# Kernel tuning notes

Measured on AMD Instinct MI355X. Metric: run time of the kernel, lower is better.

Reference implementation:

```python
import jax, jax.numpy as jnp
import numpy as np

N, T, E = 50000, 12, 800000
IN_DIM, SP_DIM, TP_DIM = 128, 128, 128


def setup_inputs() -> dict:
    key = jax.random.key(0)
    ks = jax.random.split(key, 9)
    h = jax.random.normal(ks[0], (N, T, IN_DIM), dtype=jnp.float32)
    src = jax.random.randint(ks[1], (E,), 0, N, dtype=jnp.int32)
    dst = jax.random.randint(ks[2], (E,), 0, N, dtype=jnp.int32)
    s = 1.0 / np.sqrt(IN_DIM).astype(np.float32)
    # GraphConv layer weights (xavier-ish) and zero biases, layer1: in->sp, layer2: sp->sp
    Wg1 = jax.random.normal(ks[3], (IN_DIM, SP_DIM), dtype=jnp.float32) * s
    bg1 = jnp.zeros((SP_DIM,), jnp.float32)
    Wg2 = jax.random.normal(ks[4], (SP_DIM, SP_DIM), dtype=jnp.float32) * s
    bg2 = jnp.zeros((SP_DIM,), jnp.float32)
    # LSTM params, torch layout: [4H, in]/[4H, H], gate order i,f,g,o
    t = 1.0 / np.sqrt(TP_DIM).astype(np.float32)
    w_ih = jax.random.uniform(ks[5], (4 * TP_DIM, IN_DIM), jnp.float32, -t, t)
    w_hh = jax.random.uniform(ks[6], (4 * TP_DIM, TP_DIM), jnp.float32, -t, t)
    b_ih = jax.random.uniform(ks[7], (4 * TP_DIM,), jnp.float32, -t, t)
    b_hh = jax.random.uniform(ks[8], (4 * TP_DIM,), jnp.float32, -t, t)
    return dict(h=h, src=src, dst=dst, Wg1=Wg1, bg1=bg1, Wg2=Wg2, bg2=bg2,
                w_ih=w_ih, w_hh=w_hh, b_ih=b_ih, b_hh=b_hh)


def _graph_conv(x, src, dst, norm_src, norm_dst, W, b):
    # DGL GraphConv norm='both': D_out^{-1/2} on source feats, sum-aggregate to dst,
    # D_in^{-1/2} on result, then dense weight + bias.
    x = x * norm_src                                  # [N, D]
    m = jax.ops.segment_sum(x[src], dst, num_segments=N)  # SpMM: [N, D]
    m = m * norm_dst
    return m @ W + b


def reference(h, src, dst, Wg1, bg1, Wg2, bg2, w_ih, w_hh, b_ih, b_hh):
    ones_e = jnp.ones((E,), jnp.float32)
    out_deg = jnp.maximum(jax.ops.segment_sum(ones_e, src, num_segments=N), 1.0)
    in_deg = jnp.maximum(jax.ops.segment_sum(ones_e, dst, num_segments=N), 1.0)
    norm_src = (out_deg ** -0.5)[:, None]
    norm_dst = (in_deg ** -0.5)[:, None]

    hs_list = []
    for i in range(T):  # fixed small time horizon
        x = h[:, i]  # [N, IN_DIM]
        x = jax.nn.gelu(_graph_conv(x, src, dst, norm_src, norm_dst, Wg1, bg1), approximate=False)
        x = jax.nn.gelu(_graph_conv(x, src, dst, norm_src, norm_dst, Wg2, bg2), approximate=False)
        hs_list.append(jnp.mean(x, axis=0))  # dgl.mean_nodes over the single graph
    hs = jnp.stack(hs_list, axis=0)[None]  # [1, T, SP_DIM]

    # temporal branch: LSTM over time, nodes as batch, then mean over time
    def lstm_step(carry, x_t):
        hp, cp = carry
        gates = x_t @ w_ih.T + b_ih + hp @ w_hh.T + b_hh  # [N, 4H]
        i_, f_, g_, o_ = jnp.split(gates, 4, axis=-1)
        c = jax.nn.sigmoid(f_) * cp + jax.nn.sigmoid(i_) * jnp.tanh(g_)
        ho = jax.nn.sigmoid(o_) * jnp.tanh(c)
        return (ho, c), ho

    h0 = jnp.zeros((N, TP_DIM), jnp.float32)
    _, ht_seq = jax.lax.scan(lstm_step, (h0, h0), jnp.swapaxes(h, 0, 1))  # [T, N, H]
    ht = jnp.mean(ht_seq, axis=0)  # torch.mean over dim=1 (time) -> [N, H]
    return hs, ht
```

## Files before the change

kernel.cpp:

```cpp
#include <hip/hip_runtime.h>
#include <math.h>

#define NN 50000
#define TT 12
#define EE 800000
#define DIM 128

typedef short bf16x8 __attribute__((ext_vector_type(8)));
typedef float f32x4 __attribute__((ext_vector_type(4)));

__device__ __forceinline__ float sigmoidf_(float x) { return 1.0f / (1.0f + expf(-x)); }
__device__ __forceinline__ float geluf_(float x) {
  return 0.5f * x * (1.0f + erff(x * 0.70710678118654752440f));
}
__device__ __forceinline__ unsigned short f2b(float f) {
  union { float f; unsigned u; } v;
  v.f = f;
  unsigned r = (v.u + 0x7fffu + ((v.u >> 16) & 1u)) >> 16;
  return (unsigned short)r;
}
__device__ __forceinline__ float blo(unsigned u) {
  union { unsigned x; float f; } v; v.x = u << 16; return v.f;
}
__device__ __forceinline__ float bhi(unsigned u) {
  union { unsigned x; float f; } v; v.x = u & 0xffff0000u; return v.f;
}
__device__ __forceinline__ float b2f(unsigned short b) {
  union { unsigned u; float f; } v; v.u = ((unsigned)b) << 16; return v.f;
}
__device__ __forceinline__ unsigned short f2h(float f) {
  union { _Float16 h; unsigned short s; } v; v.h = (_Float16)f; return v.s;
}
__device__ __forceinline__ float h2f(unsigned short u) {
  union { unsigned short s; _Float16 h; } v; v.s = u; return (float)v.h;
}


__global__ void deg_kernel(const int* __restrict__ src, const int* __restrict__ dst,
                           int* __restrict__ ds, int* __restrict__ dd) {
  int e = blockIdx.x * 256 + threadIdx.x;
  if (e < EE) {
    atomicAdd(&ds[src[e]], 1);
    atomicAdd(&dd[dst[e]], 1);
  }
}

__global__ void norm_kernel(const int* __restrict__ ds, const int* __restrict__ dd,
                            float* __restrict__ ns, float* __restrict__ nd) {
  int i = blockIdx.x * 256 + threadIdx.x;
  if (i < NN) {
    ns[i] = rsqrtf((float)(ds[i] > 1 ? ds[i] : 1));
    nd[i] = rsqrtf((float)(dd[i] > 1 ? dd[i] : 1));
  }
}

__global__ void scan_kernel(const int* __restrict__ cnt, int* __restrict__ row_ptr, int n) {
  __shared__ int sm[1024];
  __shared__ int carry;
  int tid = threadIdx.x;
  if (tid == 0) carry = 0;
  __syncthreads();
  for (int base = 0; base < n; base += 1024) {
    int v = (base + tid < n) ? cnt[base + tid] : 0;
    sm[tid] = v;
    __syncthreads();
    for (int off = 1; off < 1024; off <<= 1) {
      int t = (tid >= off) ? sm[tid - off] : 0;
      __syncthreads();
      sm[tid] += t;
      __syncthreads();
    }
    int incl = sm[tid];
    if (base + tid < n) row_ptr[base + tid] = carry + incl - v;
    int tot = sm[1023];
    __syncthreads();
    if (tid == 0) carry += tot;
    __syncthreads();
  }
  if (tid == 0) row_ptr[n] = carry;
}

__global__ void csr_kernel(const int* __restrict__ src, const int* __restrict__ dst,
                           const int* __restrict__ row_ptr, int* __restrict__ fill,
                           int* __restrict__ col) {
  int e = blockIdx.x * 256 + threadIdx.x;
  if (e < EE) {
    int d = dst[e];
    int pos = row_ptr[d] + atomicAdd(&fill[d], 1);
    col[pos] = src[e];
  }
}


__global__ void prep_w(const float* __restrict__ Wg1, const float* __restrict__ Wg2,
                       const float* __restrict__ wih, const float* __restrict__ whh,
                       const float* __restrict__ bih, const float* __restrict__ bhh,
                       unsigned short* __restrict__ W2bt, unsigned short* __restrict__ Wcomb,
                       unsigned short* __restrict__ whhb, float* __restrict__ bgate) {
  int i = blockIdx.x * 256 + threadIdx.x;
  if (i < 16384) {
    int n = i >> 7, k = i & 127;
    W2bt[i] = f2b(Wg2[k * 128 + n]);
  }
  int j = i - 16384;
  if (j >= 0 && j < 81920) {
    int n = j >> 7, k = j & 127;
    Wcomb[j] = f2b(n < 128 ? Wg1[k * 128 + n] : wih[(n - 128) * 128 + k]);
  }
  int q = i - (16384 + 81920);
  if (q >= 0 && q < 65536) whhb[q] = f2b(whh[q]);
  if (i < 512) bgate[i] = bih[i] + bhh[i];
}

#define LDT 40

__global__ __launch_bounds__(256) void gemm_h_all(
    const float* __restrict__ A, const float* __restrict__ ns,
    const unsigned short* __restrict__ Wcomb, unsigned short* __restrict__ C,
    unsigned short* __restrict__ xg, int M) {
  __shared__ unsigned short As[4 * 128 * LDT];
  __shared__ unsigned short Bs[128 * LDT];
  const int tid = threadIdx.x;
  const int lane = tid & 63, wid = tid >> 6;
  const int quad = lane >> 4, l16 = lane & 15;
  const int row0 = blockIdx.x * 128;
  const int wm = (wid >> 1) * 64, wn = (wid & 1) * 64;

#pragma unroll
  for (int rds = 0; rds < 8; rds++) {
    int idx = rds * 256 + tid;
    int m = idx >> 4;
    int k8 = (idx & 15) * 8;
    int gr = row0 + m;
    if (gr >= M) gr = M - 1;
    const float4 va = *(const float4*)(A + (size_t)gr * 128 + k8);
    const float4 vb = *(const float4*)(A + (size_t)gr * 128 + k8 + 4);
    int chunk = k8 >> 5, c = k8 & 31;
    unsigned short* d = &As[(chunk * 128 + m) * LDT + c];
    d[0] = f2b(va.x); d[1] = f2b(va.y); d[2] = f2b(va.z); d[3] = f2b(va.w);
    d[4] = f2b(vb.x); d[5] = f2b(vb.y); d[6] = f2b(vb.z); d[7] = f2b(vb.w);
  }

  for (int cb = 0; cb < 5; cb++) {
    f32x4 acc[4][4] = {};
#pragma unroll
    for (int k0 = 0; k0 < 4; k0++) {
      __syncthreads();
      {
        int n = tid >> 1;
        int c = (tid & 1) * 16;
        const unsigned short* srcw = Wcomb + ((size_t)(cb * 128 + n)) * 128 + k0 * 32 + c;
        *(uint4*)(&Bs[n * LDT + c]) = *(const uint4*)srcw;
        *(uint4*)(&Bs[n * LDT + c + 8]) = *(const uint4*)(srcw + 8);
      }
      __syncthreads();
      bf16x8 af[4], bfr[4];
#pragma unroll
      for (int im = 0; im < 4; im++)
        af[im] = *(const bf16x8*)(&As[(k0 * 128 + wm + im * 16 + l16) * LDT + quad * 8]);
#pragma unroll
      for (int in = 0; in < 4; in++)
        bfr[in] = *(const bf16x8*)(&Bs[(wn + in * 16 + l16) * LDT + quad * 8]);
#pragma unroll
      for (int im = 0; im < 4; im++)
#pragma unroll
        for (int in = 0; in < 4; in++)
          acc[im][in] = __builtin_amdgcn_mfma_f32_16x16x32_bf16(af[im], bfr[in], acc[im][in], 0, 0, 0);
    }
    if (cb == 0) {
#pragma unroll
      for (int im = 0; im < 4; im++)
#pragma unroll
        for (int r = 0; r < 4; r++) {
          int row = row0 + wm + im * 16 + quad * 4 + r;
          if (row < M) {
            float s = ns[row / TT];
#pragma unroll
            for (int in = 0; in < 4; in++)
              C[(size_t)row * 128 + wn + in * 16 + l16] = f2b(acc[im][in][r] * s);
          }
        }
    } else {
      const int goff = (cb - 1) * 128;
#pragma unroll
      for (int im = 0; im < 4; im++)
#pragma unroll
        for (int r = 0; r < 4; r++) {
          int row = row0 + wm + im * 16 + quad * 4 + r;
          if (row < M)
#pragma unroll
            for (int in = 0; in < 4; in++)
              xg[(size_t)row * 512 + goff + wn + in * 16 + l16] = f2h(acc[im][in][r]);
        }
    }
  }
}

__global__ __launch_bounds__(256) void gemm_bf16A(
    const unsigned short* __restrict__ A, const unsigned short* __restrict__ Bt,
    unsigned short* __restrict__ C, int M) {
  __shared__ unsigned short As[128 * LDT];
  __shared__ unsigned short Bs[128 * LDT];
  const int tid = threadIdx.x;
  const int lane = tid & 63, wid = tid >> 6;
  const int quad = lane >> 4, l16 = lane & 15;
  const int row0 = blockIdx.x * 128;
  const int wm = (wid >> 1) * 64, wn = (wid & 1) * 64;
  f32x4 acc[4][4] = {};
  for (int k0 = 0; k0 < 128; k0 += 32) {
#pragma unroll
    for (int rds = 0; rds < 2; rds++) {
      int idx = (rds * 256 + tid) * 8;
      int m = idx >> 5, c = idx & 31;
      int gr = row0 + m;
      if (gr >= M) gr = M - 1;
      *(uint4*)(&As[m * LDT + c]) = *(const uint4*)(A + (size_t)gr * 128 + k0 + c);
      *(uint4*)(&Bs[m * LDT + c]) = *(const uint4*)(Bt + m * 128 + k0 + c);
    }
    __syncthreads();
    bf16x8 af[4], bfr[4];
#pragma unroll
    for (int im = 0; im < 4; im++)
      af[im] = *(const bf16x8*)(&As[(wm + im * 16 + l16) * LDT + quad * 8]);
#pragma unroll
    for (int in = 0; in < 4; in++)
      bfr[in] = *(const bf16x8*)(&Bs[(wn + in * 16 + l16) * LDT + quad * 8]);
#pragma unroll
    for (int im = 0; im < 4; im++)
#pragma unroll
      for (int in = 0; in < 4; in++)
        acc[im][in] = __builtin_amdgcn_mfma_f32_16x16x32_bf16(af[im], bfr[in], acc[im][in], 0, 0, 0);
    __syncthreads();
  }
#pragma unroll
  for (int im = 0; im < 4; im++)
#pragma unroll
    for (int r = 0; r < 4; r++) {
      int row = row0 + wm + im * 16 + quad * 4 + r;
      if (row < M)
#pragma unroll
        for (int in = 0; in < 4; in++)
          C[(size_t)row * 128 + wn + in * 16 + l16] = f2b(acc[im][in][r]);
    }
}


template <bool SCALE_OUT>
__global__ __launch_bounds__(256) void spmm_b(
    const unsigned short* __restrict__ z, const int* __restrict__ rowp,
    const int* __restrict__ colx, const float* __restrict__ ns,
    const float* __restrict__ nd, const float* __restrict__ bg,
    unsigned short* __restrict__ y) {
  int d = (blockIdx.x * 256 + threadIdx.x) >> 6;
  int lane = threadIdx.x & 63;
  if (d >= NN) return;
  int beg = rowp[d], end = rowp[d + 1];
  float acc[3][8] = {};
  int j = beg;
  int s = (j < end) ? colx[j] : 0;
  while (j < end) {
    int snext = (j + 1 < end) ? colx[j + 1] : 0;
    const unsigned short* base = z + (size_t)s * 1536 + lane * 8;
#pragma unroll
    for (int r = 0; r < 3; r++) {
      uint4 v = *(const uint4*)(base + r * 512);
      acc[r][0] += blo(v.x); acc[r][1] += bhi(v.x);
      acc[r][2] += blo(v.y); acc[r][3] += bhi(v.y);
      acc[r][4] += blo(v.z); acc[r][5] += bhi(v.z);
      acc[r][6] += blo(v.w); acc[r][7] += bhi(v.w);
    }
    s = snext;
    j++;
  }
  float scn = nd[d];
  float sco = SCALE_OUT ? ns[d] : 1.0f;
  float bgv[8];
#pragma unroll
  for (int k = 0; k < 8; k++) bgv[k] = bg[(lane * 8 + k) & 127];
  unsigned short* outp = y + (size_t)d * 1536 + lane * 8;
#pragma unroll
  for (int r = 0; r < 3; r++) {
    unsigned short o[8];
#pragma unroll
    for (int k = 0; k < 8; k++)
      o[k] = f2b(sco * geluf_(acc[r][k] * scn + bgv[k]));
    *(uint4*)(outp + r * 512) = *(const uint4*)o;
  }
}


__global__ void colmean_b(const unsigned short* __restrict__ x, float* __restrict__ out) {
  int t = blockIdx.x;
  int cc = threadIdx.x & 127;
  int half = threadIdx.x >> 7;
  float s = 0.f;
  for (int n = blockIdx.y * 2 + half; n < NN; n += 64)
    s += b2f(x[((size_t)n * TT + t) * 128 + cc]);
  __shared__ float sm[256];
  sm[threadIdx.x] = s;
  __syncthreads();
  if (threadIdx.x < 128)
    atomicAdd(&out[t * 128 + cc], (sm[threadIdx.x] + sm[threadIdx.x + 128]) * (1.0f / NN));
}

#define HPLD 136
#define WLD 136

__global__ __launch_bounds__(512, 2) void lstm_hh(
    const unsigned short* __restrict__ whhb, const unsigned short* __restrict__ xg,
    const float* __restrict__ bgate, float* __restrict__ ht_out, int M) {
  __shared__ unsigned short Ws[512 * WLD];
  __shared__ unsigned short Hp[64 * HPLD];
  const int tid = threadIdx.x;
  const int lane = tid & 63;
  const int w = tid >> 6;
  const int quad = lane >> 4, l16 = lane & 15;
  const int row0 = blockIdx.x * 64;
  const int colg = w * 16 + l16;

#pragma unroll
  for (int it = 0; it < 16; it++) {
    int idx = it * 512 + tid;
    int n = idx >> 4, c = (idx & 15) * 8;
    *(uint4*)(&Ws[n * WLD + c]) = *(const uint4*)(whhb + n * 128 + c);
  }

  float cs[4][4], hacc[4][4];
#pragma unroll
  for (int im = 0; im < 4; im++)
#pragma unroll
    for (int r = 0; r < 4; r++) { cs[im][r] = 0.f; hacc[im][r] = 0.f; }

  const float bi = bgate[colg], bff = bgate[128 + colg];
  const float bgg = bgate[256 + colg], bo = bgate[384 + colg];
  __syncthreads();

  for (int t = 0; t < TT; t++) {
    unsigned short xsv[4][4][4];
#pragma unroll
    for (int im = 0; im < 4; im++)
#pragma unroll
      for (int r = 0; r < 4; r++) {
        int gr = row0 + im * 16 + quad * 4 + r;
        int grc = gr < M ? gr : M - 1;
        const unsigned short* xp = xg + ((size_t)grc * TT + t) * 512 + colg;
#pragma unroll
        for (int g = 0; g < 4; g++) xsv[im][r][g] = xp[g * 128];
      }

    f32x4 acc[4][4] = {};
    if (t) {
#pragma unroll
      for (int k0 = 0; k0 < 128; k0 += 32) {
        bf16x8 af[4];
#pragma unroll
        for (int im = 0; im < 4; im++)
          af[im] = *(const bf16x8*)(&Hp[(im * 16 + l16) * HPLD + k0 + quad * 8]);
#pragma unroll
        for (int g = 0; g < 4; g++) {
          bf16x8 bf = *(const bf16x8*)(&Ws[(g * 128 + colg) * WLD + k0 + quad * 8]);
#pragma unroll
          for (int im = 0; im < 4; im++)
            acc[im][g] = __builtin_amdgcn_mfma_f32_16x16x32_bf16(af[im], bf, acc[im][g], 0, 0, 0);
        }
      }
      __syncthreads();
    }

#pragma unroll
    for (int im = 0; im < 4; im++)
#pragma unroll
      for (int r = 0; r < 4; r++) {
        float iv = sigmoidf_(acc[im][0][r] + h2f(xsv[im][r][0]) + bi);
        float fv = sigmoidf_(acc[im][1][r] + h2f(xsv[im][r][1]) + bff);
        float gv = tanhf(acc[im][2][r] + h2f(xsv[im][r][2]) + bgg);
        float ov = sigmoidf_(acc[im][3][r] + h2f(xsv[im][r][3]) + bo);
        float cn = fv * cs[im][r] + iv * gv;
        cs[im][r] = cn;
        float ho = ov * tanhf(cn);
        hacc[im][r] += ho;
        Hp[(im * 16 + quad * 4 + r) * HPLD + colg] = f2b(ho);
      }
    __syncthreads();
  }
#pragma unroll
  for (int im = 0; im < 4; im++)
#pragma unroll
    for (int r = 0; r < 4; r++) {
      int gr = row0 + im * 16 + quad * 4 + r;
      if (gr < M) ht_out[(size_t)gr * 128 + colg] = hacc[im][r] * (1.0f / TT);
    }
}


extern "C" void kernel_launch(void* const* d_in, const int* in_sizes, int n_in,
                              void* d_out, int out_size, void* d_ws, size_t ws_size,
                              hipStream_t stream) {
  const float* h   = (const float*)d_in[0];
  const int*   src = (const int*)d_in[1];
  const int*   dst = (const int*)d_in[2];
  const float* Wg1 = (const float*)d_in[3];
  const float* bg1 = (const float*)d_in[4];
  const float* Wg2 = (const float*)d_in[5];
  const float* bg2 = (const float*)d_in[6];
  const float* wih = (const float*)d_in[7];
  const float* whh = (const float*)d_in[8];
  const float* bih = (const float*)d_in[9];
  const float* bhh = (const float*)d_in[10];

  float* out = (float*)d_out;
  float* hs_out = out;
  float* ht_out = out + TT * DIM;

  char* p = (char*)d_ws;
  auto alloc = [&](size_t bytes) -> void* {
    void* r = (void*)p;
    p += (bytes + 255) & ~(size_t)255;
    return r;
  };
  const size_t MB = (size_t)NN * TT * DIM;
  unsigned short* bufA = (unsigned short*)alloc(MB * 2);
  unsigned short* bufB = (unsigned short*)alloc(MB * 2);
  unsigned short* xgb  = (unsigned short*)alloc((size_t)NN * TT * 512 * 2);
  unsigned short* W2bt = (unsigned short*)alloc(16384 * 2);
  unsigned short* Wcomb= (unsigned short*)alloc(81920 * 2);
  unsigned short* whhb = (unsigned short*)alloc(65536 * 2);
  float* bgate = (float*)alloc(512 * 4);
  float* ns    = (float*)alloc(NN * 4);
  float* nd    = (float*)alloc(NN * 4);
  int* degs    = (int*)alloc(NN * 4);
  int* degd    = (int*)alloc(NN * 4);
  int* rowp    = (int*)alloc((NN + 1) * 4);
  int* colx    = (int*)alloc(EE * 4);

  hipMemsetAsync(degs, 0, NN * 4, stream);
  hipMemsetAsync(degd, 0, NN * 4, stream);
  hipMemsetAsync(hs_out, 0, TT * DIM * 4, stream);

  deg_kernel<<<(EE + 255) / 256, 256, 0, stream>>>(src, dst, degs, degd);
  norm_kernel<<<(NN + 255) / 256, 256, 0, stream>>>(degs, degd, ns, nd);
  scan_kernel<<<1, 1024, 0, stream>>>(degd, rowp, NN);
  hipMemsetAsync(degs, 0, NN * 4, stream);
  csr_kernel<<<(EE + 255) / 256, 256, 0, stream>>>(src, dst, rowp, degs, colx);
  prep_w<<<(16384 + 81920 + 65536 + 255) / 256, 256, 0, stream>>>(
      Wg1, Wg2, wih, whh, bih, bhh, W2bt, Wcomb, whhb, bgate);

  const int M = NN * TT;
  const int gblocks = (M + 127) / 128;
  const int sblocks = (NN + 3) / 4;

  gemm_h_all<<<gblocks, 256, 0, stream>>>(h, ns, Wcomb, bufA, xgb, M);
  spmm_b<true><<<sblocks, 256, 0, stream>>>(bufA, rowp, colx, ns, nd, bg1, bufB);
  gemm_bf16A<<<gblocks, 256, 0, stream>>>(bufB, W2bt, bufA, M);
  spmm_b<false><<<sblocks, 256, 0, stream>>>(bufA, rowp, colx, ns, nd, bg2, bufB);
  colmean_b<<<dim3(TT, 32), 256, 0, stream>>>(bufB, hs_out);

  lstm_hh<<<(NN + 63) / 64, 512, 0, stream>>>(whhb, xgb, bgate, ht_out, NN);
}
```

Before: 2.442 ms.

## Keep LSTM recurrent weights in registers and use fast exp2/rcp activations

Each wave now loads its slice of W_hh into registers once, as 16 bf16x8 fragments, instead of staging the full 512x128 matrix in LDS. This shrinks shared memory per block sharply and removes the per-step LDS weight reads. The gate xg loads are moved after the MFMA block so they can overlap with it. Sigmoid and tanh are replaced by exp2/rcp intrinsic forms, which cuts transcendental cost but raises register pressure and lowers accuracy slightly.

```diff
diff --git a/kernel.cpp b/kernel.cpp
--- a/kernel.cpp
+++ b/kernel.cpp
@@ -12,6 +12,13 @@
 __device__ __forceinline__ float sigmoidf_(float x) { return 1.0f / (1.0f + expf(-x)); }
 __device__ __forceinline__ float geluf_(float x) {
   return 0.5f * x * (1.0f + erff(x * 0.70710678118654752440f));
+}
+#define LOG2E 1.44269504088896340736f
+__device__ __forceinline__ float fsigmoid(float x) {
+  return __builtin_amdgcn_rcpf(1.0f + __builtin_amdgcn_exp2f(-LOG2E * x));
+}
+__device__ __forceinline__ float ftanh(float x) {
+  return 1.0f - 2.0f * __builtin_amdgcn_rcpf(1.0f + __builtin_amdgcn_exp2f((2.0f * LOG2E) * x));
 }
 __device__ __forceinline__ unsigned short f2b(float f) {
   union { float f; unsigned u; } v;
@@ -304,12 +311,10 @@
 }
 
 #define HPLD 136
-#define WLD 136
 
 __global__ __launch_bounds__(512, 2) void lstm_hh(
     const unsigned short* __restrict__ whhb, const unsigned short* __restrict__ xg,
     const float* __restrict__ bgate, float* __restrict__ ht_out, int M) {
-  __shared__ unsigned short Ws[512 * WLD];
   __shared__ unsigned short Hp[64 * HPLD];
   const int tid = threadIdx.x;
   const int lane = tid & 63;
@@ -318,12 +323,12 @@
   const int row0 = blockIdx.x * 64;
   const int colg = w * 16 + l16;
 
-#pragma unroll
-  for (int it = 0; it < 16; it++) {
-    int idx = it * 512 + tid;
-    int n = idx >> 4, c = (idx & 15) * 8;
-    *(uint4*)(&Ws[n * WLD + c]) = *(const uint4*)(whhb + n * 128 + c);
-  }
+  bf16x8 bw[4][4];
+#pragma unroll
+  for (int g = 0; g < 4; g++)
+#pragma unroll
+    for (int k0 = 0; k0 < 4; k0++)
+      bw[g][k0] = *(const bf16x8*)(whhb + ((size_t)(g * 128 + colg)) * 128 + k0 * 32 + quad * 8);
 
   float cs[4][4], hacc[4][4];
 #pragma unroll
@@ -333,9 +338,24 @@
 
   const float bi = bgate[colg], bff = bgate[128 + colg];
   const float bgg = bgate[256 + colg], bo = bgate[384 + colg];
-  __syncthreads();
 
   for (int t = 0; t < TT; t++) {
+    f32x4 acc[4][4] = {};
+    if (t) {
+#pragma unroll
+      for (int k0 = 0; k0 < 4; k0++) {
+        bf16x8 af[4];
+#pragma unroll
+        for (int im = 0; im < 4; im++)
+          af[im] = *(const bf16x8*)(&Hp[(im * 16 + l16) * HPLD + k0 * 32 + quad * 8]);
+#pragma unroll
+        for (int g = 0; g < 4; g++)
+#pragma unroll
+          for (int im = 0; im < 4; im++)
+            acc[im][g] = __builtin_amdgcn_mfma_f32_16x16x32_bf16(af[im], bw[g][k0], acc[im][g], 0, 0, 0);
+      }
+    }
+
     unsigned short xsv[4][4][4];
 #pragma unroll
     for (int im = 0; im < 4; im++)
@@ -348,36 +368,19 @@
         for (int g = 0; g < 4; g++) xsv[im][r][g] = xp[g * 128];
       }
 
-    f32x4 acc[4][4] = {};
-    if (t) {
-#pragma unroll
-      for (int k0 = 0; k0 < 128; k0 += 32) {
-        bf16x8 af[4];
-#pragma unroll
-        for (int im = 0; im < 4; im++)
-          af[im] = *(const bf16x8*)(&Hp[(im * 16 + l16) * HPLD + k0 + quad * 8]);
-#pragma unroll
-        for (int g = 0; g < 4; g++) {
-          bf16x8 bf = *(const bf16x8*)(&Ws[(g * 128 + colg) * WLD + k0 + quad * 8]);
-#pragma unroll
-          for (int im = 0; im < 4; im++)
-            acc[im][g] = __builtin_amdgcn_mfma_f32_16x16x32_bf16(af[im], bf, acc[im][g], 0, 0, 0);
-        }
-      }
-      __syncthreads();
-    }
+    if (t) __syncthreads();
 
 #pragma unroll
     for (int im = 0; im < 4; im++)
 #pragma unroll
       for (int r = 0; r < 4; r++) {
-        float iv = sigmoidf_(acc[im][0][r] + h2f(xsv[im][r][0]) + bi);
-        float fv = sigmoidf_(acc[im][1][r] + h2f(xsv[im][r][1]) + bff);
-        float gv = tanhf(acc[im][2][r] + h2f(xsv[im][r][2]) + bgg);
-        float ov = sigmoidf_(acc[im][3][r] + h2f(xsv[im][r][3]) + bo);
+        float iv = fsigmoid(acc[im][0][r] + h2f(xsv[im][r][0]) + bi);
+        float fv = fsigmoid(acc[im][1][r] + h2f(xsv[im][r][1]) + bff);
+        float gv = ftanh(acc[im][2][r] + h2f(xsv[im][r][2]) + bgg);
+        float ov = fsigmoid(acc[im][3][r] + h2f(xsv[im][r][3]) + bo);
         float cn = fv * cs[im][r] + iv * gv;
         cs[im][r] = cn;
-        float ho = ov * tanhf(cn);
+        float ho = ov * ftanh(cn);
         hacc[im][r] += ho;
         Hp[(im * 16 + quad * 4 + r) * HPLD + colg] = f2b(ho);
       }
```

After: 2.313 ms. 1.06x faster.
